# Kernel tuning notes

Hardware: AMD Instinct MI355X
Metric: run time of the kernel (lower is better)

## Reference

```python
import jax, jax.numpy as jnp
import numpy as np

IN_DIM = 4096
OUT_DIM = 4096
CODEBOOK_SIZE = 65536
LAYER_ID = 3
HASH_A, HASH_B, HASH_C = 10007, 20011, 40009
SIGN_HASH_A, SIGN_HASH_B, SIGN_HASH_C = 4099, 6151, 14887
SIGNED_HASH = True
BATCH = 8192


def _hash_tables():
    i = jnp.arange(OUT_DIM, dtype=jnp.int64 if jax.config.jax_enable_x64 else jnp.int32)[:, None]
    j = jnp.arange(IN_DIM, dtype=i.dtype)[None, :]
    idx = (i * HASH_A + j * HASH_B + LAYER_ID * HASH_C) % CODEBOOK_SIZE
    bits = (i * SIGN_HASH_A + j * SIGN_HASH_B + LAYER_ID * SIGN_HASH_C) % 2
    signs = bits.astype(jnp.float32) * 2.0 - 1.0
    return idx, signs


def setup_inputs() -> dict:
    key = jax.random.key(0)
    kx, kc = jax.random.split(key)
    x = jax.random.normal(kx, (BATCH, IN_DIM), dtype=jnp.float32)
    codebook = jax.random.normal(kc, (CODEBOOK_SIZE,), dtype=jnp.float32) * 0.01
    bias = jnp.zeros((OUT_DIM,), dtype=jnp.float32)
    return {"x": x, "codebook": codebook, "bias": bias}


def reference(x, codebook, bias):
    idx, signs = _hash_tables()  # [out_dim, in_dim] each
    weight = codebook[idx]  # gather from tiny codebook -> [out_dim, in_dim]
    if SIGNED_HASH:
        weight = weight * signs.astype(weight.dtype)
    # F.linear: y = x @ W^T + b
    return jnp.einsum('bi,oi->bo', x, weight) + bias
```

## Files before the change

### kernel.cpp

```cpp
#include <hip/hip_runtime.h>
#include <hip/hip_bf16.h>

constexpr int M_ = 8192;
constexpr int N_ = 4096;
constexpr int K_ = 4096;
constexpr int CBOOK = 65536;
constexpr int HA = 10007, HB = 20011;
constexpr int HC3 = 3 * 40009;

constexpr int BM = 128, BN = 128, BK = 64;

using bf16x8 = __bf16 __attribute__((ext_vector_type(8)));
using f32x4  = float __attribute__((ext_vector_type(4)));
using u16x8  = unsigned short __attribute__((ext_vector_type(8)));

typedef __attribute__((address_space(3))) void lds_void_t;
typedef const __attribute__((address_space(1))) void gbl_void_t;

static __device__ __forceinline__ unsigned short f2bf(float f) {
    __bf16 h = (__bf16)f;
    return __builtin_bit_cast(unsigned short, h);
}

constexpr int GENB  = N_ * K_ / 8 / 256;
constexpr int CONVB = M_ * K_ / 8 / 256;

__global__ __launch_bounds__(256) void prep_kernel(const float* __restrict__ x,
                                                   const float* __restrict__ cb,
                                                   unsigned short* __restrict__ W,
                                                   unsigned short* __restrict__ xb) {
    const int b = blockIdx.x;
    if (b < GENB) {
        const int t  = b * 256 + threadIdx.x;
        const int o  = t >> 9;
        const int ib = (t & 511) << 3;
        const int h  = o * HA + ib * HB + HC3;
        u16x8 out;
#pragma unroll
        for (int j = 0; j < 8; ++j) {
            const int idx = (h + j * HB) & (CBOOK - 1);
            float v = cb[idx];
            v = ((o ^ (ib + j)) & 1) ? -v : v;
            out[j] = f2bf(v);
        }
        *reinterpret_cast<u16x8*>(&W[(size_t)o * K_ + ib]) = out;
    } else {
        const size_t t = (size_t)(b - GENB) * 256 + threadIdx.x;
        const float4* p = reinterpret_cast<const float4*>(x) + t * 2;
        const float4 a = p[0], c = p[1];
        u16x8 out;
        out[0] = f2bf(a.x); out[1] = f2bf(a.y); out[2] = f2bf(a.z); out[3] = f2bf(a.w);
        out[4] = f2bf(c.x); out[5] = f2bf(c.y); out[6] = f2bf(c.z); out[7] = f2bf(c.w);
        reinterpret_cast<u16x8*>(xb)[t] = out;
    }
}

__global__ __launch_bounds__(256) void gemm_kernel(const unsigned short* __restrict__ A,
                                                   const unsigned short* __restrict__ W,
                                                   const float* __restrict__ bias,
                                                   float* __restrict__ C) {
    __shared__ __align__(16) unsigned short ldsA[BM * BK];
    __shared__ __align__(16) unsigned short ldsB[BN * BK];

    const int tid  = threadIdx.x;
    const int lane = tid & 63;
    const int wv   = tid >> 6;
    const int wm   = wv >> 1;
    const int wn   = wv & 1;
    const int m0 = blockIdx.y * BM;
    const int n0 = blockIdx.x * BN;

    const int quad = lane >> 4;
    const int l16  = lane & 15;
    const int lr = lane >> 3;
    const int lc = lane & 7;
    const int scol = (lc ^ lr) * 8;
    const int sw   = l16 & 7;

    f32x4 acc[4][4] = {};

    for (int k0 = 0; k0 < K_; k0 += BK) {
        {
            const unsigned short* gA = A + (size_t)m0 * K_ + k0;
            const unsigned short* gB = W + (size_t)n0 * K_ + k0;
#pragma unroll
            for (int r = 0; r < 4; ++r) {
                const int rowb = wv * 32 + r * 8;
                const unsigned short* srcA = gA + (size_t)(rowb + lr) * K_ + scol;
                const unsigned short* srcB = gB + (size_t)(rowb + lr) * K_ + scol;
                __builtin_amdgcn_global_load_lds((gbl_void_t*)srcA,
                                                 (lds_void_t*)&ldsA[rowb * BK], 16, 0, 0);
                __builtin_amdgcn_global_load_lds((gbl_void_t*)srcB,
                                                 (lds_void_t*)&ldsB[rowb * BK], 16, 0, 0);
            }
        }
        __syncthreads();

#pragma unroll
        for (int kk = 0; kk < 2; ++kk) {
            bf16x8 af[4], bfr[4];
            const int blk = ((kk * 4 + quad) ^ sw) * 8;
#pragma unroll
            for (int mt = 0; mt < 4; ++mt)
                af[mt] = *reinterpret_cast<const bf16x8*>(
                    &ldsA[(wm * 64 + mt * 16 + l16) * BK + blk]);
#pragma unroll
            for (int nt = 0; nt < 4; ++nt)
                bfr[nt] = *reinterpret_cast<const bf16x8*>(
                    &ldsB[(wn * 64 + nt * 16 + l16) * BK + blk]);
#pragma unroll
            for (int mt = 0; mt < 4; ++mt)
#pragma unroll
                for (int nt = 0; nt < 4; ++nt)
                    acc[mt][nt] = __builtin_amdgcn_mfma_f32_16x16x32_bf16(
                        af[mt], bfr[nt], acc[mt][nt], 0, 0, 0);
        }
        __syncthreads();
    }

#pragma unroll
    for (int nt = 0; nt < 4; ++nt) {
        const int col = n0 + wn * 64 + nt * 16 + l16;
        const float bv = bias[col];
#pragma unroll
        for (int mt = 0; mt < 4; ++mt) {
            const int rowb = m0 + wm * 64 + mt * 16 + quad * 4;
#pragma unroll
            for (int r = 0; r < 4; ++r)
                C[(size_t)(rowb + r) * N_ + col] = acc[mt][nt][r] + bv;
        }
    }
}

__global__ __launch_bounds__(256) void naive_kernel(const float* __restrict__ x,
                                                    const float* __restrict__ cb,
                                                    const float* __restrict__ bias,
                                                    float* __restrict__ out) {
    const size_t t = (size_t)blockIdx.x * 256 + threadIdx.x;
    const int row = (int)(t / N_);
    const int col = (int)(t % N_);
    float s = bias[col];
    const float* xr = x + (size_t)row * K_;
    const int h = col * HA + HC3;
    for (int i = 0; i < K_; ++i) {
        float v = cb[(h + i * HB) & (CBOOK - 1)];
        s += xr[i] * (((col ^ i) & 1) ? -v : v);
    }
    out[t] = s;
}

extern "C" void kernel_launch(void* const* d_in, const int* in_sizes, int n_in,
                              void* d_out, int out_size, void* d_ws, size_t ws_size,
                              hipStream_t stream) {
    const float* x    = (const float*)d_in[0];
    const float* cb   = (const float*)d_in[1];
    const float* bias = (const float*)d_in[2];
    float* out = (float*)d_out;

    const size_t wBytes = (size_t)N_ * K_ * sizeof(unsigned short);
    const size_t xBytes = (size_t)M_ * K_ * sizeof(unsigned short);

    if (ws_size >= wBytes + xBytes) {
        unsigned short* W  = (unsigned short*)d_ws;
        unsigned short* xb = (unsigned short*)((char*)d_ws + wBytes);
        prep_kernel<<<GENB + CONVB, 256, 0, stream>>>(x, cb, W, xb);
        gemm_kernel<<<dim3(N_ / BN, M_ / BM), 256, 0, stream>>>(xb, W, bias, out);
    } else {
        naive_kernel<<<(int)((size_t)M_ * N_ / 256), 256, 0, stream>>>(x, cb, bias, out);
    }
}
```

Measured before the change: 542.7 us.

## Pre-swizzle weights into MFMA fragment layout and stream A with double-buffered LDS

The prep kernel now writes the generated bf16 weights directly in MFMA fragment order, so each lane of the GEMM loads its B fragments straight from global memory without staging them in LDS. The GEMM tile grows to 256x128: each wave owns 64 rows across all 128 columns, with 4x8 accumulators. Only A goes through LDS, now double-buffered so the next K tile is prefetched while the current one is consumed, which drops one barrier per iteration. The cost is more registers per wave (accumulators plus 16 B fragments, with launch bounds asking for 2 blocks per CU) and B reads that are exposed global-memory latency with no LDS reuse across waves.

```diff
diff --git a/kernel.cpp b/kernel.cpp
--- a/kernel.cpp
+++ b/kernel.cpp
@@ -8,7 +8,8 @@
 constexpr int HA = 10007, HB = 20011;
 constexpr int HC3 = 3 * 40009;
 
-constexpr int BM = 128, BN = 128, BK = 64;
+constexpr int BM = 256, BN = 128, BK = 64;
+constexpr int KITERS = K_ / BK;
 
 using bf16x8 = __bf16 __attribute__((ext_vector_type(8)));
 using f32x4  = float __attribute__((ext_vector_type(4)));
@@ -27,23 +28,26 @@
 
 __global__ __launch_bounds__(256) void prep_kernel(const float* __restrict__ x,
                                                    const float* __restrict__ cb,
-                                                   unsigned short* __restrict__ W,
+                                                   unsigned short* __restrict__ Wf,
                                                    unsigned short* __restrict__ xb) {
     const int b = blockIdx.x;
     if (b < GENB) {
-        const int t  = b * 256 + threadIdx.x;
-        const int o  = t >> 9;
-        const int ib = (t & 511) << 3;
-        const int h  = o * HA + ib * HB + HC3;
+        const int t     = b * 256 + threadIdx.x;
+        const int lane  = t & 63;
+        const int ktile = (t >> 6) & 127;
+        const int ntile = t >> 13;
+        const int n  = (ntile << 4) + (lane & 15);
+        const int kb = (ktile << 5) + ((lane >> 4) << 3);
+        const int h  = n * HA + kb * HB + HC3;
         u16x8 out;
 #pragma unroll
         for (int j = 0; j < 8; ++j) {
             const int idx = (h + j * HB) & (CBOOK - 1);
             float v = cb[idx];
-            v = ((o ^ (ib + j)) & 1) ? -v : v;
+            v = ((n ^ (kb + j)) & 1) ? -v : v;
             out[j] = f2bf(v);
         }
-        *reinterpret_cast<u16x8*>(&W[(size_t)o * K_ + ib]) = out;
+        *reinterpret_cast<u16x8*>(&Wf[(size_t)t * 8]) = out;
     } else {
         const size_t t = (size_t)(b - GENB) * 256 + threadIdx.x;
         const float4* p = reinterpret_cast<const float4*>(x) + t * 2;
@@ -55,18 +59,16 @@
     }
 }
 
-__global__ __launch_bounds__(256) void gemm_kernel(const unsigned short* __restrict__ A,
-                                                   const unsigned short* __restrict__ W,
-                                                   const float* __restrict__ bias,
-                                                   float* __restrict__ C) {
-    __shared__ __align__(16) unsigned short ldsA[BM * BK];
-    __shared__ __align__(16) unsigned short ldsB[BN * BK];
+__global__ __launch_bounds__(256, 2) void gemm_kernel(
+        const unsigned short* __restrict__ A,
+        const unsigned short* __restrict__ Wf,
+        const float* __restrict__ bias,
+        float* __restrict__ C) {
+    __shared__ __align__(16) unsigned short ldsA[2][BM * BK];
 
     const int tid  = threadIdx.x;
     const int lane = tid & 63;
     const int wv   = tid >> 6;
-    const int wm   = wv >> 1;
-    const int wn   = wv & 1;
     const int m0 = blockIdx.y * BM;
     const int n0 = blockIdx.x * BN;
 
@@ -77,54 +79,67 @@
     const int scol = (lc ^ lr) * 8;
     const int sw   = l16 & 7;
 
-    f32x4 acc[4][4] = {};
+    const unsigned short* aLane = A + (size_t)(m0 + lr) * K_ + scol;
+    const unsigned short* wLane = Wf + (size_t)lane * 8;
+    const int ntile0 = n0 >> 4;
 
-    for (int k0 = 0; k0 < K_; k0 += BK) {
-        {
-            const unsigned short* gA = A + (size_t)m0 * K_ + k0;
-            const unsigned short* gB = W + (size_t)n0 * K_ + k0;
+    f32x4 acc[4][8] = {};
+
 #pragma unroll
-            for (int r = 0; r < 4; ++r) {
-                const int rowb = wv * 32 + r * 8;
-                const unsigned short* srcA = gA + (size_t)(rowb + lr) * K_ + scol;
-                const unsigned short* srcB = gB + (size_t)(rowb + lr) * K_ + scol;
-                __builtin_amdgcn_global_load_lds((gbl_void_t*)srcA,
-                                                 (lds_void_t*)&ldsA[rowb * BK], 16, 0, 0);
-                __builtin_amdgcn_global_load_lds((gbl_void_t*)srcB,
-                                                 (lds_void_t*)&ldsB[rowb * BK], 16, 0, 0);
+    for (int r = 0; r < 8; ++r) {
+        const int rowb = wv * 64 + r * 8;
+        __builtin_amdgcn_global_load_lds(
+            (gbl_void_t*)(aLane + (size_t)rowb * K_),
+            (lds_void_t*)&ldsA[0][rowb * BK], 16, 0, 0);
+    }
+
+    for (int i = 0; i < KITERS; ++i) {
+        __syncthreads();
+        const int buf = i & 1;
+
+        if (i + 1 < KITERS) {
+            const unsigned short* aNext = aLane + (size_t)(i + 1) * BK;
+#pragma unroll
+            for (int r = 0; r < 8; ++r) {
+                const int rowb = wv * 64 + r * 8;
+                __builtin_amdgcn_global_load_lds(
+                    (gbl_void_t*)(aNext + (size_t)rowb * K_),
+                    (lds_void_t*)&ldsA[buf ^ 1][rowb * BK], 16, 0, 0);
             }
         }
-        __syncthreads();
+
+        bf16x8 bfr[2][8];
+#pragma unroll
+        for (int kk = 0; kk < 2; ++kk)
+#pragma unroll
+            for (int nt = 0; nt < 8; ++nt)
+                bfr[kk][nt] = *reinterpret_cast<const bf16x8*>(
+                    wLane + (((size_t)(ntile0 + nt) << 7) + i * 2 + kk) * 512);
 
 #pragma unroll
         for (int kk = 0; kk < 2; ++kk) {
-            bf16x8 af[4], bfr[4];
+            bf16x8 af[4];
             const int blk = ((kk * 4 + quad) ^ sw) * 8;
 #pragma unroll
             for (int mt = 0; mt < 4; ++mt)
                 af[mt] = *reinterpret_cast<const bf16x8*>(
-                    &ldsA[(wm * 64 + mt * 16 + l16) * BK + blk]);
-#pragma unroll
-            for (int nt = 0; nt < 4; ++nt)
-                bfr[nt] = *reinterpret_cast<const bf16x8*>(
-                    &ldsB[(wn * 64 + nt * 16 + l16) * BK + blk]);
+                    &ldsA[buf][(wv * 64 + mt * 16 + l16) * BK + blk]);
 #pragma unroll
             for (int mt = 0; mt < 4; ++mt)
 #pragma unroll
-                for (int nt = 0; nt < 4; ++nt)
+                for (int nt = 0; nt < 8; ++nt)
                     acc[mt][nt] = __builtin_amdgcn_mfma_f32_16x16x32_bf16(
-                        af[mt], bfr[nt], acc[mt][nt], 0, 0, 0);
+                        af[mt], bfr[kk][nt], acc[mt][nt], 0, 0, 0);
         }
-        __syncthreads();
     }
 
 #pragma unroll
-    for (int nt = 0; nt < 4; ++nt) {
-        const int col = n0 + wn * 64 + nt * 16 + l16;
+    for (int nt = 0; nt < 8; ++nt) {
+        const int col = n0 + nt * 16 + l16;
         const float bv = bias[col];
 #pragma unroll
         for (int mt = 0; mt < 4; ++mt) {
-            const int rowb = m0 + wm * 64 + mt * 16 + quad * 4;
+            const int rowb = m0 + wv * 64 + mt * 16 + quad * 4;
 #pragma unroll
             for (int r = 0; r < 4; ++r)
                 C[(size_t)(rowb + r) * N_ + col] = acc[mt][nt][r] + bv;
@@ -161,10 +176,10 @@
     const size_t xBytes = (size_t)M_ * K_ * sizeof(unsigned short);
 
     if (ws_size >= wBytes + xBytes) {
-        unsigned short* W  = (unsigned short*)d_ws;
+        unsigned short* Wf = (unsigned short*)d_ws;
         unsigned short* xb = (unsigned short*)((char*)d_ws + wBytes);
-        prep_kernel<<<GENB + CONVB, 256, 0, stream>>>(x, cb, W, xb);
-        gemm_kernel<<<dim3(N_ / BN, M_ / BM), 256, 0, stream>>>(xb, W, bias, out);
+        prep_kernel<<<GENB + CONVB, 256, 0, stream>>>(x, cb, Wf, xb);
+        gemm_kernel<<<dim3(N_ / BN, M_ / BM), 256, 0, stream>>>(xb, Wf, bias, out);
     } else {
         naive_kernel<<<(int)((size_t)M_ * N_ / 256), 256, 0, stream>>>(x, cb, bias, out);
     }
```

Measured after the change: 524.9 us. 1.03x faster.
